# Performance work log

Measured on AMD Instinct MI355X. Metric: run time of the kernel, lower is better.

## Reference

```python
import jax, jax.numpy as jnp
import numpy as np
from itertools import combinations_with_replacement

IN_FEATURES = 128
ORDER = 3
BIAS = True
WEIGHT_DIVISOR = 100.0
BATCH = 256


def _make_comb_idx():
    n_feat = IN_FEATURES + (1 if BIAS else 0)  # 129
    idx = np.array(list(combinations_with_replacement(range(n_feat), ORDER)), dtype=np.int32)
    return jnp.asarray(idx)  # [num_combinations, ORDER] = [366145, 3]


def setup_inputs() -> dict:
    key = jax.random.key(0)
    kx, kw = jax.random.split(key)
    x = jax.random.normal(kx, (BATCH, IN_FEATURES), dtype=jnp.float32)
    comb_idx = _make_comb_idx()
    num_weights = comb_idx.shape[0]
    weight = jax.random.uniform(kw, (num_weights,), dtype=jnp.float32) / WEIGHT_DIVISOR
    return {"x": x, "weight": weight, "comb_idx": comb_idx}


def reference(x, weight, comb_idx):
    # Prepend bias column of ones: xb [B, in_features+1]
    ones = jnp.ones((x.shape[0], 1), dtype=x.dtype)
    xb = jnp.concatenate([ones, x], axis=1)
    # Gather per-combination features: [B, num_combinations, ORDER]
    gathered = xb[:, comb_idx]
    # Monomial products: [B, num_combinations]
    colx = jnp.prod(gathered, axis=2)
    # Weighted sum -> [B, 1]; activation is identity
    return colx @ weight[:, None]
```

## Files before the change

kernel.cpp:

```cpp
#include <hip/hip_runtime.h>


#define NF      129
#define NCOMB   366145
#define NPAIR   8385
#define NT      4
#define NCHUNK  132
#define NKS     4

typedef short bf16x8 __attribute__((ext_vector_type(8)));
typedef float f32x4  __attribute__((ext_vector_type(4)));

union i4b8 { int4 i; bf16x8 b; };

static __device__ inline unsigned bfpack2(float lo, float hi) {
    union { float f; unsigned u; } a, b; a.f = lo; b.f = hi;
    return ((b.u + 0x8000u) & 0xffff0000u) | ((a.u + 0x8000u) >> 16);
}

static __device__ inline void dpair(int p, int& i0, int& i1) {
    int t = (int)((259.0f - sqrtf((float)(67081 - 8 * p))) * 0.5f);
    t = t < 0 ? 0 : (t > 128 ? 128 : t);
    while (t < 128 && ((t + 1) * (258 - t)) / 2 <= p) ++t;
    while (t > 0   && (t * (259 - t)) / 2      >  p) --t;
    i0 = t; i1 = t + (p - (t * (259 - t)) / 2);
}

static __device__ inline int mbase(int i0, int i1) {
    const int n0 = NF - i0, n1 = NF - i1;
    return NCOMB - (n0 * (n0 + 1) * (n0 + 2)) / 6
                 + ((n0 * (n0 + 1)) >> 1) - ((n1 * (n1 + 1)) >> 1);
}

__global__ __launch_bounds__(256, 3) void honu_fused(const float* __restrict__ x,
                                                     const float* __restrict__ w,
                                                     float* __restrict__ out) {
    __shared__ float  xf[64 * NF];
    __shared__ bf16x8 wls[NT * NKS * 64];
    __shared__ int4   dec[64];

    const int tid  = threadIdx.x;
    const int lane = tid & 63;
    const int wv   = tid >> 6;
    const int bx   = blockIdx.x;
    const int by   = blockIdx.y;

    {
        const int r = tid >> 2, q = tid & 3;
        const float4* xr = (const float4*)(x + (size_t)(by * 64 + r) * 128);
        #pragma unroll
        for (int t = 0; t < 8; ++t) {
            const int c4 = q + 4 * t;
            const float4 v = xr[c4];
            float* d = &xf[r * NF + 1 + 4 * c4];
            d[0] = v.x; d[1] = v.y; d[2] = v.z; d[3] = v.w;
        }
        if (tid < 64) xf[tid * NF] = 1.0f;
    }

    if (tid < 64) {
        const int p = bx * 64 + tid;
        int i0 = 0, i1 = 200, mb = 0; unsigned wl = 0;
        if (p < NPAIR) {
            dpair(p, i0, i1);
            mb = mbase(i0, i1);
            union { float f; unsigned u; } c; c.f = w[mb + 128 - i1];
            wl = c.u;
        }
        dec[tid] = make_int4(i0 | (i1 << 16), mb, (int)wl, 0);
    }
    __syncthreads();

    #pragma unroll
    for (int it = 0; it < 4; ++it) {
        const int item = tid + it * 256;
        const int pl = item >> 4, r = item & 15;
        const int4 pd = dec[pl];
        const int i1 = pd.x >> 16;
        const int mb = pd.y;
        const int k0 = r * 8;
        int4 vout = make_int4(0, 0, 0, 0);
        if (k0 + 7 >= i1) {
            float f[8];
            #pragma unroll
            for (int j = 0; j < 8; ++j) {
                const int k = k0 + j;
                int off = k - i1; off = off < 0 ? 0 : off;
                const float t = w[mb + off];
                f[j] = (k >= i1) ? t : 0.0f;
            }
            vout.x = (int)bfpack2(f[0], f[1]);
            vout.y = (int)bfpack2(f[2], f[3]);
            vout.z = (int)bfpack2(f[4], f[5]);
            vout.w = (int)bfpack2(f[6], f[7]);
        }
        const int nt = pl >> 4, s = r >> 2;
        const int slane = ((r & 3) << 4) | (pl & 15);
        ((int4*)wls)[(nt * NKS + s) * 64 + slane] = vout;
    }

    const int am = wv * 16 + (lane & 15);
    const int aq = (lane >> 4) * 8;
    const float* xa = &xf[am * NF + aq];
    bf16x8 a[NKS];
    #pragma unroll
    for (int s = 0; s < NKS; ++s) {
        const float* p = xa + s * 32;
        i4b8 av;
        av.i.x = (int)bfpack2(p[0], p[1]);
        av.i.y = (int)bfpack2(p[2], p[3]);
        av.i.z = (int)bfpack2(p[4], p[5]);
        av.i.w = (int)bfpack2(p[6], p[7]);
        a[s] = av.b;
    }
    __syncthreads();

    const int lr0 = wv * 16 + (lane >> 4) * 4;
    const float* r0 = &xf[lr0 * NF];
    float o0 = 0.f, o1 = 0.f, o2 = 0.f, o3 = 0.f;

    #pragma unroll
    for (int nt = 0; nt < NT; ++nt) {
        f32x4 acc = {0.f, 0.f, 0.f, 0.f};
        #pragma unroll
        for (int s = 0; s < NKS; ++s)
            acc = __builtin_amdgcn_mfma_f32_16x16x32_bf16(
                      a[s], wls[(nt * NKS + s) * 64 + lane], acc, 0, 0, 0);

        const int4 pd = dec[nt * 16 + (lane & 15)];
        const int i0 = pd.x & 0xffff;
        int i1 = pd.x >> 16; if (i1 > 128) i1 = 0;
        union { int i; float f; } wc; wc.i = pd.z;
        const float wl = wc.f;
        o0 = fmaf(acc[0] + r0[128]          * wl, r0[i0]          * r0[i1],          o0);
        o1 = fmaf(acc[1] + r0[NF + 128]     * wl, r0[NF + i0]     * r0[NF + i1],     o1);
        o2 = fmaf(acc[2] + r0[2 * NF + 128] * wl, r0[2 * NF + i0] * r0[2 * NF + i1], o2);
        o3 = fmaf(acc[3] + r0[3 * NF + 128] * wl, r0[3 * NF + i0] * r0[3 * NF + i1], o3);
    }

    #pragma unroll
    for (int msk = 1; msk < 16; msk <<= 1) {
        o0 += __shfl_xor(o0, msk);
        o1 += __shfl_xor(o1, msk);
        o2 += __shfl_xor(o2, msk);
        o3 += __shfl_xor(o3, msk);
    }
    if ((lane & 15) == 0) {
        float* po = out + by * 64 + lr0;
        atomicAdd(po + 0, o0);
        atomicAdd(po + 1, o1);
        atomicAdd(po + 2, o2);
        atomicAdd(po + 3, o3);
    }
}

extern "C" void kernel_launch(void* const* d_in, const int* in_sizes, int n_in,
                              void* d_out, int out_size, void* d_ws, size_t ws_size,
                              hipStream_t stream) {
    const float* x      = (const float*)d_in[0];
    const float* weight = (const float*)d_in[1];
    float* out = (float*)d_out;

    hipMemsetAsync(out, 0, out_size, stream);

    honu_fused<<<dim3(NCHUNK, 4), 256, 0, stream>>>(x, weight, out);
}
```

Baseline: 79.63 us.

## Split weight expansion into a separate kernel and DMA tiles into LDS

Moves the per-pair weight gather, bf16 packing and pair decoding out of the main kernel into a preceding expansion kernel that runs once instead of once per batch block. The MFMA kernel then loads the pre-laid-out weight tiles directly into shared memory with global_load_lds and reads a compact decode table. This removes fourfold redundant scattered gathers at the cost of an extra launch and a write/read round trip through workspace memory.

```diff
diff --git a/kernel.cpp b/kernel.cpp
--- a/kernel.cpp
+++ b/kernel.cpp
@@ -7,6 +7,8 @@
 #define NT      4
 #define NCHUNK  132
 #define NKS     4
+#define NGROUP  (NCHUNK * 4)
+#define DEC_OFF (4u << 20)
 
 typedef short bf16x8 __attribute__((ext_vector_type(8)));
 typedef float f32x4  __attribute__((ext_vector_type(4)));
@@ -32,18 +34,64 @@
                  + ((n0 * (n0 + 1)) >> 1) - ((n1 * (n1 + 1)) >> 1);
 }
 
-__global__ __launch_bounds__(256, 3) void honu_fused(const float* __restrict__ x,
-                                                     const float* __restrict__ w,
-                                                     float* __restrict__ out) {
-    __shared__ float  xf[64 * NF];
-    __shared__ bf16x8 wls[NT * NKS * 64];
-    __shared__ int4   dec[64];
+__global__ __launch_bounds__(256) void honu_expand(const float* __restrict__ w,
+                                                   int4* __restrict__ wexp,
+                                                   int2* __restrict__ dec2) {
+    const int item = blockIdx.x * 256 + threadIdx.x;
+    const int n = item & 15, q = (item >> 4) & 3, s = (item >> 6) & 3, g = item >> 8;
+    const int p = g * 16 + n;
+    int4 vout = make_int4(0, 0, 0, 0);
+    if (p < NPAIR) {
+        int i0, i1; dpair(p, i0, i1);
+        const int mb = mbase(i0, i1);
+        const int k0 = s * 32 + q * 8;
+        if (k0 + 7 >= i1) {
+            float f[8];
+            #pragma unroll
+            for (int j = 0; j < 8; ++j) {
+                const int k = k0 + j;
+                int off = k - i1; off = off < 0 ? 0 : off;
+                const float t = w[mb + off];
+                f[j] = (k >= i1) ? t : 0.0f;
+            }
+            vout.x = (int)bfpack2(f[0], f[1]);
+            vout.y = (int)bfpack2(f[2], f[3]);
+            vout.z = (int)bfpack2(f[4], f[5]);
+            vout.w = (int)bfpack2(f[6], f[7]);
+        }
+        if ((item & 0xF0) == 0) {
+            union { float f; unsigned u; } c; c.f = w[mb + 128 - i1];
+            dec2[p] = make_int2(i0 | (i1 << 16), (int)c.u);
+        }
+    } else if ((item & 0xF0) == 0) {
+        dec2[p] = make_int2(200 << 16, 0);
+    }
+    wexp[item] = vout;
+}
+
+__global__ __launch_bounds__(256, 3) void honu_mfma(const float* __restrict__ x,
+                                                    const int4* __restrict__ wexp,
+                                                    const int2* __restrict__ dec2g,
+                                                    float* __restrict__ out) {
+    __shared__ float xf[64 * NF];
+    __shared__ int4  wls[NT * NKS * 64];
+    __shared__ int2  dec[64];
 
     const int tid  = threadIdx.x;
     const int lane = tid & 63;
     const int wv   = tid >> 6;
     const int bx   = blockIdx.x;
     const int by   = blockIdx.y;
+
+    #pragma unroll
+    for (int it = 0; it < 4; ++it) {
+        const int seg = it * 4 + wv;
+        const int4* gp = wexp + (size_t)bx * 1024 + seg * 64 + lane;
+        __builtin_amdgcn_global_load_lds(
+            (const __attribute__((address_space(1))) void*)gp,
+            (__attribute__((address_space(3))) void*)((char*)wls + seg * 1024),
+            16, 0, 0);
+    }
 
     {
         const int r = tid >> 2, q = tid & 3;
@@ -58,46 +106,8 @@
         if (tid < 64) xf[tid * NF] = 1.0f;
     }
 
-    if (tid < 64) {
-        const int p = bx * 64 + tid;
-        int i0 = 0, i1 = 200, mb = 0; unsigned wl = 0;
-        if (p < NPAIR) {
-            dpair(p, i0, i1);
-            mb = mbase(i0, i1);
-            union { float f; unsigned u; } c; c.f = w[mb + 128 - i1];
-            wl = c.u;
-        }
-        dec[tid] = make_int4(i0 | (i1 << 16), mb, (int)wl, 0);
-    }
+    if (tid < 64) dec[tid] = dec2g[bx * 64 + tid];
     __syncthreads();
-
-    #pragma unroll
-    for (int it = 0; it < 4; ++it) {
-        const int item = tid + it * 256;
-        const int pl = item >> 4, r = item & 15;
-        const int4 pd = dec[pl];
-        const int i1 = pd.x >> 16;
-        const int mb = pd.y;
-        const int k0 = r * 8;
-        int4 vout = make_int4(0, 0, 0, 0);
-        if (k0 + 7 >= i1) {
-            float f[8];
-            #pragma unroll
-            for (int j = 0; j < 8; ++j) {
-                const int k = k0 + j;
-                int off = k - i1; off = off < 0 ? 0 : off;
-                const float t = w[mb + off];
-                f[j] = (k >= i1) ? t : 0.0f;
-            }
-            vout.x = (int)bfpack2(f[0], f[1]);
-            vout.y = (int)bfpack2(f[2], f[3]);
-            vout.z = (int)bfpack2(f[4], f[5]);
-            vout.w = (int)bfpack2(f[6], f[7]);
-        }
-        const int nt = pl >> 4, s = r >> 2;
-        const int slane = ((r & 3) << 4) | (pl & 15);
-        ((int4*)wls)[(nt * NKS + s) * 64 + slane] = vout;
-    }
 
     const int am = wv * 16 + (lane & 15);
     const int aq = (lane >> 4) * 8;
@@ -117,6 +127,7 @@
 
     const int lr0 = wv * 16 + (lane >> 4) * 4;
     const float* r0 = &xf[lr0 * NF];
+    const bf16x8* wb = (const bf16x8*)wls;
     float o0 = 0.f, o1 = 0.f, o2 = 0.f, o3 = 0.f;
 
     #pragma unroll
@@ -125,12 +136,12 @@
         #pragma unroll
         for (int s = 0; s < NKS; ++s)
             acc = __builtin_amdgcn_mfma_f32_16x16x32_bf16(
-                      a[s], wls[(nt * NKS + s) * 64 + lane], acc, 0, 0, 0);
+                      a[s], wb[(nt * NKS + s) * 64 + lane], acc, 0, 0, 0);
 
-        const int4 pd = dec[nt * 16 + (lane & 15)];
+        const int2 pd = dec[nt * 16 + (lane & 15)];
         const int i0 = pd.x & 0xffff;
         int i1 = pd.x >> 16; if (i1 > 128) i1 = 0;
-        union { int i; float f; } wc; wc.i = pd.z;
+        union { int i; float f; } wc; wc.i = pd.y;
         const float wl = wc.f;
         o0 = fmaf(acc[0] + r0[128]          * wl, r0[i0]          * r0[i1],          o0);
         o1 = fmaf(acc[1] + r0[NF + 128]     * wl, r0[NF + i0]     * r0[NF + i1],     o1);
@@ -159,9 +170,12 @@
                               hipStream_t stream) {
     const float* x      = (const float*)d_in[0];
     const float* weight = (const float*)d_in[1];
-    float* out = (float*)d_out;
+    float* out  = (float*)d_out;
+    int4*  wexp = (int4*)d_ws;
+    int2*  dec2 = (int2*)((char*)d_ws + DEC_OFF);
 
     hipMemsetAsync(out, 0, out_size, stream);
 
-    honu_fused<<<dim3(NCHUNK, 4), 256, 0, stream>>>(x, weight, out);
+    honu_expand<<<NGROUP, 256, 0, stream>>>(weight, wexp, dec2);
+    honu_mfma<<<dim3(NCHUNK, 4), 256, 0, stream>>>(x, wexp, dec2, out);
 }
```

New measurement: 80.50 us. About the same (+1.1%).

## Merge batch blocks into 1024-thread blocks and replace atomics with two-pass reduction

Applied to the files above, without the earlier changes.

Each block now covers all 256 batch rows with 1024 threads instead of splitting the batch across grid.y, so the pair weights are decoded and staged in shared memory once per chunk instead of four times. Pair decoding for the weight load is recomputed per thread, which shrinks the dec table. Per-block partial sums go to a workspace and a second kernel reduces them, replacing the memset and the float atomics. The cost is an extra kernel launch, one block per CU with about 130KB of LDS, and reliance on the workspace being large enough.

```diff
diff --git a/kernel.cpp b/kernel.cpp
--- a/kernel.cpp
+++ b/kernel.cpp
@@ -7,6 +7,7 @@
 #define NT      4
 #define NCHUNK  132
 #define NKS     4
+#define NPW     132
 
 typedef short bf16x8 __attribute__((ext_vector_type(8)));
 typedef float f32x4  __attribute__((ext_vector_type(4)));
@@ -32,22 +33,21 @@
                  + ((n0 * (n0 + 1)) >> 1) - ((n1 * (n1 + 1)) >> 1);
 }
 
-__global__ __launch_bounds__(256, 3) void honu_fused(const float* __restrict__ x,
-                                                     const float* __restrict__ w,
-                                                     float* __restrict__ out) {
-    __shared__ float  xf[64 * NF];
+__global__ __launch_bounds__(1024, 1) void honu_fused2(const float* __restrict__ x,
+                                                       const float* __restrict__ w,
+                                                       float* __restrict__ part) {
+    __shared__ float  xf[256 * NF];
     __shared__ bf16x8 wls[NT * NKS * 64];
-    __shared__ int4   dec[64];
+    __shared__ int2   dec[64];
 
     const int tid  = threadIdx.x;
     const int lane = tid & 63;
     const int wv   = tid >> 6;
     const int bx   = blockIdx.x;
-    const int by   = blockIdx.y;
 
     {
         const int r = tid >> 2, q = tid & 3;
-        const float4* xr = (const float4*)(x + (size_t)(by * 64 + r) * 128);
+        const float4* xr = (const float4*)(x + (size_t)r * 128);
         #pragma unroll
         for (int t = 0; t < 8; ++t) {
             const int c4 = q + 4 * t;
@@ -55,32 +55,32 @@
             float* d = &xf[r * NF + 1 + 4 * c4];
             d[0] = v.x; d[1] = v.y; d[2] = v.z; d[3] = v.w;
         }
-        if (tid < 64) xf[tid * NF] = 1.0f;
+        if (tid < 256) xf[tid * NF] = 1.0f;
     }
 
     if (tid < 64) {
         const int p = bx * 64 + tid;
-        int i0 = 0, i1 = 200, mb = 0; unsigned wl = 0;
+        int i0 = 0, i1 = 200; unsigned wl = 0;
         if (p < NPAIR) {
-            dpair(p, i0, i1);
+            int mb; dpair(p, i0, i1);
             mb = mbase(i0, i1);
             union { float f; unsigned u; } c; c.f = w[mb + 128 - i1];
             wl = c.u;
         }
-        dec[tid] = make_int4(i0 | (i1 << 16), mb, (int)wl, 0);
+        dec[tid] = make_int2(i0 | (i1 << 16), (int)wl);
     }
     __syncthreads();
 
-    #pragma unroll
-    for (int it = 0; it < 4; ++it) {
-        const int item = tid + it * 256;
-        const int pl = item >> 4, r = item & 15;
-        const int4 pd = dec[pl];
+    {
+        const int pl = tid >> 4, r = tid & 15;
+        const int2 pd = dec[pl];
         const int i1 = pd.x >> 16;
-        const int mb = pd.y;
         const int k0 = r * 8;
         int4 vout = make_int4(0, 0, 0, 0);
         if (k0 + 7 >= i1) {
+            const int p = bx * 64 + pl;
+            int a0, a1; dpair(p, a0, a1);
+            const int mb = mbase(a0, a1);
             float f[8];
             #pragma unroll
             for (int j = 0; j < 8; ++j) {
@@ -127,10 +127,10 @@
             acc = __builtin_amdgcn_mfma_f32_16x16x32_bf16(
                       a[s], wls[(nt * NKS + s) * 64 + lane], acc, 0, 0, 0);
 
-        const int4 pd = dec[nt * 16 + (lane & 15)];
+        const int2 pd = dec[nt * 16 + (lane & 15)];
         const int i0 = pd.x & 0xffff;
         int i1 = pd.x >> 16; if (i1 > 128) i1 = 0;
-        union { int i; float f; } wc; wc.i = pd.z;
+        union { int i; float f; } wc; wc.i = pd.y;
         const float wl = wc.f;
         o0 = fmaf(acc[0] + r0[128]          * wl, r0[i0]          * r0[i1],          o0);
         o1 = fmaf(acc[1] + r0[NF + 128]     * wl, r0[NF + i0]     * r0[NF + i1],     o1);
@@ -146,12 +146,23 @@
         o3 += __shfl_xor(o3, msk);
     }
     if ((lane & 15) == 0) {
-        float* po = out + by * 64 + lr0;
-        atomicAdd(po + 0, o0);
-        atomicAdd(po + 1, o1);
-        atomicAdd(po + 2, o2);
-        atomicAdd(po + 3, o3);
+        float* pp = part + (size_t)lr0 * NPW + bx;
+        pp[0]       = o0;
+        pp[NPW]     = o1;
+        pp[2 * NPW] = o2;
+        pp[3 * NPW] = o3;
     }
+}
+
+__global__ __launch_bounds__(256) void honu_reduce(const float* __restrict__ part,
+                                                   float* __restrict__ out) {
+    const int lane = threadIdx.x & 63;
+    const int r = blockIdx.x * 4 + (threadIdx.x >> 6);
+    const float* pr = part + (size_t)r * NPW;
+    float s = pr[lane] + pr[64 + lane] + (lane < 4 ? pr[128 + lane] : 0.f);
+    #pragma unroll
+    for (int m = 32; m >= 1; m >>= 1) s += __shfl_xor(s, m);
+    if (lane == 0) out[r] = s;
 }
 
 extern "C" void kernel_launch(void* const* d_in, const int* in_sizes, int n_in,
@@ -159,9 +170,9 @@
                               hipStream_t stream) {
     const float* x      = (const float*)d_in[0];
     const float* weight = (const float*)d_in[1];
-    float* out = (float*)d_out;
+    float* out  = (float*)d_out;
+    float* part = (float*)d_ws;
 
-    hipMemsetAsync(out, 0, out_size, stream);
-
-    honu_fused<<<dim3(NCHUNK, 4), 256, 0, stream>>>(x, weight, out);
+    honu_fused2<<<NCHUNK, 1024, 0, stream>>>(x, weight, part);
+    honu_reduce<<<64, 256, 0, stream>>>(part, out);
 }
```

New measurement: 68.42 us. -14.1%, faster.
